# Kernel tuning notes

Measured on AMD Instinct MI355X. Metric: run time of the kernel, lower is better.

Reference implementation:

```python
import jax, jax.numpy as jnp
import numpy as np


def _add_self_loops(edge_index, num_nodes):
    loops = jnp.arange(num_nodes, dtype=edge_index.dtype)
    row = jnp.concatenate([edge_index[0], loops])
    col = jnp.concatenate([edge_index[1], loops])
    return row, col


def _gcn_norm(row, col, num_nodes):
    # deg computed at aggregation targets (col), edge weights all 1 (PyG gcn_norm)
    deg = jax.ops.segment_sum(jnp.ones_like(col, dtype=jnp.float32), col,
                              num_segments=num_nodes)
    dinv = jnp.where(deg > 0, jax.lax.rsqrt(deg), 0.0)
    return dinv[row] * dinv[col]  # [E+N]


def _gcn_conv(x, row, col, norm, W, b, num_nodes):
    h = x @ W                                  # [N, out] linear first (PyG GCNConv)
    msg = h[row] * norm[:, None]               # gather + scale, [E+N, out]
    agg = jax.ops.segment_sum(msg, col, num_segments=num_nodes)
    return agg + b


def setup_inputs() -> dict:
    key = jax.random.key(0)
    N, F, H, E = 100000, 128, 64, 1600000
    k1, k2, k3, k4 = jax.random.split(key, 4)
    x = jax.random.normal(k1, (N, F), dtype=jnp.float32)
    edge_index = jax.random.randint(k2, (2, E), 0, N, dtype=jnp.int64)
    s1 = 1.0 / np.sqrt(F)
    s2 = 1.0 / np.sqrt(H)
    W1 = jax.random.normal(k3, (F, H), dtype=jnp.float32) * s1
    b1 = jnp.zeros((H,), dtype=jnp.float32)
    W2 = jax.random.normal(k4, (H, 1), dtype=jnp.float32) * s2
    b2 = jnp.zeros((1,), dtype=jnp.float32)
    return {"x": x, "edge_index": edge_index, "W1": W1, "b1": b1,
            "W2": W2, "b2": b2}


def reference(x, edge_index, W1, b1, W2, b2):
    N = x.shape[0]
    row, col = _add_self_loops(edge_index, N)
    norm = _gcn_norm(row, col, N)
    h = jax.nn.relu(_gcn_conv(x, row, col, norm, W1, b1, N))
    # dropout p=0.0 -> identity
    out = _gcn_conv(h, row, col, norm, W2, b2, N)
    return out.reshape(-1)  # [N]
```

## Files before the change

kernel.cpp:

```cpp
#include <hip/hip_runtime.h>
#include <hip/hip_bf16.h>


#define SHIFT 9
#define BMASK ((1 << SHIFT) - 1)

typedef __attribute__((ext_vector_type(8))) short bf16x8;
typedef __attribute__((ext_vector_type(4))) float f32x4;

__device__ __forceinline__ bool detect_i64(const unsigned* u) {
    unsigned acc = 0;
#pragma unroll
    for (int i = 1; i <= 32; ++i) acc |= u[2 * i + 1];
    return acc == 0u;
}

__device__ __forceinline__ int load_edge(const void* ei, bool is64, long long idx) {
    if (is64) return ((const int*)ei)[idx << 1];
    return ((const int*)ei)[idx];
}

__device__ __forceinline__ unsigned bf16_rn(float x) {
    unsigned u = __float_as_uint(x);
    return (u + 0x7fffu + ((u >> 16) & 1u)) >> 16;
}
__device__ __forceinline__ unsigned pack_bf2(float a, float b) {
    return bf16_rn(a) | (bf16_rn(b) << 16);
}
__device__ __forceinline__ float bflo(unsigned v) { return __uint_as_float(v << 16); }
__device__ __forceinline__ float bfhi(unsigned v) {
    return __uint_as_float(v & 0xffff0000u);
}

__global__ __launch_bounds__(256) void binA_kernel(const void* ei, int* gcursor,
                                                   unsigned* __restrict__ pairs, int E,
                                                   int cap) {
    bool is64 = detect_i64((const unsigned*)ei);
    __shared__ int whist[4][256];
    __shared__ int bcur[256];
    int t = threadIdx.x;
    int wid = t >> 6;
    long long per = ((long long)E + gridDim.x - 1) / gridDim.x;
    long long e0 = (long long)blockIdx.x * per;
    long long e1 = e0 + per;
    if (e1 > E) e1 = E;
    whist[0][t] = 0; whist[1][t] = 0; whist[2][t] = 0; whist[3][t] = 0;
    __syncthreads();
    for (long long e = e0 + t; e < e1; e += 256) {
        int c = load_edge(ei, is64, (long long)E + e);
        atomicAdd(&whist[wid][c >> SHIFT], 1);
    }
    __syncthreads();
    int tot = whist[0][t] + whist[1][t] + whist[2][t] + whist[3][t];
    int rel = tot ? atomicAdd(&gcursor[t], tot) : 0;
    bcur[t] = t * cap + rel;
    __syncthreads();
    for (long long e = e0 + t; e < e1; e += 256) {
        int r = load_edge(ei, is64, e);
        int c = load_edge(ei, is64, (long long)E + e);
        int b = c >> SHIFT;
        int rk = atomicAdd(&bcur[b], 1);
        pairs[rk] = ((unsigned)r << SHIFT) | (unsigned)(c & BMASK);
    }
}

__global__ __launch_bounds__(256) void binB_kernel(const unsigned* __restrict__ pairs,
                                                   const int* __restrict__ gcursor,
                                                   int* __restrict__ csr,
                                                   int* __restrict__ offs,
                                                   int* __restrict__ deg, int N,
                                                   int cap) {
    __shared__ int cnt[1 << SHIFT];
    __shared__ int cur[1 << SHIFT];
    __shared__ int tmp[256];
    int b = blockIdx.x, t = threadIdx.x;
    int start = b * cap, end = b * cap + gcursor[b];
    cnt[t] = 0;
    cnt[t + 256] = 0;
    __syncthreads();
    for (int i = start + t; i < end; i += 256) atomicAdd(&cnt[pairs[i] & BMASK], 1);
    __syncthreads();
    int c0 = cnt[2 * t], c1 = cnt[2 * t + 1];
    int s = c0 + c1;
    tmp[t] = s;
    __syncthreads();
    for (int off = 1; off < 256; off <<= 1) {
        int xv = (t >= off) ? tmp[t - off] : 0;
        __syncthreads();
        tmp[t] += xv;
        __syncthreads();
    }
    int excl = tmp[t] - s;
    int p0 = start + excl;
    int p1 = p0 + c0;
    cur[2 * t] = p0;
    cur[2 * t + 1] = p1;
    int node0 = (b << SHIFT) + 2 * t;
    if (node0 < N) { offs[node0] = p0; deg[node0] = c0; }
    if (node0 + 1 < N) { offs[node0 + 1] = p1; deg[node0 + 1] = c1; }
    __syncthreads();
    for (int i = start + t; i < end; i += 256) {
        unsigned p = pairs[i];
        int pos = atomicAdd(&cur[p & BMASK], 1);
        csr[pos] = (int)(p >> SHIFT);
    }
}

__global__ __launch_bounds__(256) void gemm1_kernel(const float* __restrict__ x,
                                                    const float* __restrict__ W1,
                                                    const int* __restrict__ deg,
                                                    unsigned* __restrict__ hs_u, int N) {
    __shared__ alignas(16) char smem[32768];
    char* wt_hi = smem;
    char* wt_lo = smem + 16384;
    int t = threadIdx.x;
    int l = t & 63;
    int w = t >> 6;

#pragma unroll
    for (int i = 0; i < 32; ++i) {
        int idx = t + 256 * i;
        int k = idx >> 6;
        int c = idx & 63;
        float f = W1[idx];
        unsigned uh = bf16_rn(f);
        float fh = __uint_as_float(uh << 16);
        unsigned ul = bf16_rn(f - fh);
        int byte = c * 256 + (((k >> 3) ^ (c & 15)) << 4) + ((k & 7) << 1);
        *(unsigned short*)(wt_hi + byte) = (unsigned short)uh;
        *(unsigned short*)(wt_lo + byte) = (unsigned short)ul;
    }
    __syncthreads();

    int row0 = blockIdx.x * 64 + w * 16;
    int arow = row0 + (l & 15);
    bool rok = arow < N;
    const f32x4* x4 = (const f32x4*)x;

    f32x4 acc[4];
#pragma unroll
    for (int ct = 0; ct < 4; ++ct) acc[ct] = (f32x4)(0.f);

#pragma unroll
    for (int ks = 0; ks < 4; ++ks) {
        int kbase = ks * 32 + (l >> 4) * 8;
        f32x4 xa = (f32x4)(0.f), xb = (f32x4)(0.f);
        if (rok) {
            xa = x4[(size_t)arow * 32 + (kbase >> 2)];
            xb = x4[(size_t)arow * 32 + (kbase >> 2) + 1];
        }
        unsigned ah[4], al[4];
#pragma unroll
        for (int j = 0; j < 4; ++j) {
            float f0 = (j < 2) ? ((j == 0) ? xa.x : xa.z) : ((j == 2) ? xb.x : xb.z);
            float f1 = (j < 2) ? ((j == 0) ? xa.y : xa.w) : ((j == 2) ? xb.y : xb.w);
            unsigned h0 = bf16_rn(f0), h1 = bf16_rn(f1);
            float r0 = f0 - __uint_as_float(h0 << 16);
            float r1 = f1 - __uint_as_float(h1 << 16);
            ah[j] = h0 | (h1 << 16);
            al[j] = bf16_rn(r0) | (bf16_rn(r1) << 16);
        }
        bf16x8 Ah, Al;
        ((unsigned*)&Ah)[0] = ah[0]; ((unsigned*)&Ah)[1] = ah[1];
        ((unsigned*)&Ah)[2] = ah[2]; ((unsigned*)&Ah)[3] = ah[3];
        ((unsigned*)&Al)[0] = al[0]; ((unsigned*)&Al)[1] = al[1];
        ((unsigned*)&Al)[2] = al[2]; ((unsigned*)&Al)[3] = al[3];
        int chunk = ks * 4 + (l >> 4);
#pragma unroll
        for (int ct = 0; ct < 4; ++ct) {
            int col = ct * 16 + (l & 15);
            int byte = col * 256 + ((chunk ^ (col & 15)) << 4);
            bf16x8 Bh = *(const bf16x8*)(wt_hi + byte);
            bf16x8 Bl = *(const bf16x8*)(wt_lo + byte);
            acc[ct] = __builtin_amdgcn_mfma_f32_16x16x32_bf16(Ah, Bh, acc[ct], 0, 0, 0);
            acc[ct] = __builtin_amdgcn_mfma_f32_16x16x32_bf16(Ah, Bl, acc[ct], 0, 0, 0);
            acc[ct] = __builtin_amdgcn_mfma_f32_16x16x32_bf16(Al, Bh, acc[ct], 0, 0, 0);
        }
    }

    __syncthreads();
    float* hsb = (float*)(smem) + w * 16 * 68;
#pragma unroll
    for (int ct = 0; ct < 4; ++ct) {
#pragma unroll
        for (int i = 0; i < 4; ++i) {
            int row = (l >> 4) * 4 + i;
            hsb[row * 68 + ct * 16 + (l & 15)] = acc[ct][i];
        }
    }
    __syncthreads();
    int row = l & 15;
    int q = l >> 4;
    int gr = row0 + row;
    if (gr < N) {
        float dinv = rsqrtf((float)deg[gr] + 1.0f);
        const f32x4* src = (const f32x4*)(hsb + row * 68 + q * 16);
        f32x4 f0 = src[0], f1 = src[1], f2 = src[2], f3 = src[3];
        uint4 o0, o1;
        o0.x = pack_bf2(f0.x * dinv, f0.y * dinv);
        o0.y = pack_bf2(f0.z * dinv, f0.w * dinv);
        o0.z = pack_bf2(f1.x * dinv, f1.y * dinv);
        o0.w = pack_bf2(f1.z * dinv, f1.w * dinv);
        o1.x = pack_bf2(f2.x * dinv, f2.y * dinv);
        o1.y = pack_bf2(f2.z * dinv, f2.w * dinv);
        o1.z = pack_bf2(f3.x * dinv, f3.y * dinv);
        o1.w = pack_bf2(f3.z * dinv, f3.w * dinv);
        uint4* dst = (uint4*)&hs_u[(size_t)gr * 32 + q * 8];
        dst[0] = o0;
        dst[1] = o1;
    }
}

#define ACCV(v)                                            \
    {                                                      \
        float2 t0 = make_float2(bflo((v).x), bfhi((v).x)); \
        float2 t1 = make_float2(bflo((v).y), bfhi((v).y)); \
        float2 t2 = make_float2(bflo((v).z), bfhi((v).z)); \
        float2 t3 = make_float2(bflo((v).w), bfhi((v).w)); \
        a0.x += t0.x; a0.y += t0.y;                        \
        a1.x += t1.x; a1.y += t1.y;                        \
        a2.x += t2.x; a2.y += t2.y;                        \
        a3.x += t3.x; a3.y += t3.y;                        \
    }

__global__ __launch_bounds__(256) void pull1_kernel(
    const uint4* __restrict__ hs4, const int* __restrict__ offs,
    const int* __restrict__ deg, const int* __restrict__ csr,
    const float* __restrict__ b1, const float* __restrict__ W2,
    float* __restrict__ hs2, int N) {
    int gid = blockIdx.x * blockDim.x + threadIdx.x;
    int w = gid >> 3;
    if (w >= N) return;
    int lane = threadIdx.x & 63;
    int k = lane & 7;
    int s = offs[w];
    int cnt = deg[w];
    float dinv = rsqrtf((float)cnt + 1.0f);
    float2 a0 = make_float2(0.f, 0.f), a1 = a0, a2 = a0, a3 = a0;
    {
        uint4 v = hs4[(size_t)w * 8 + k];
        ACCV(v);
    }
    int e = 0;
    for (; e + 8 <= cnt; e += 8) {
        int r0 = csr[s + e + 0];
        int r1 = csr[s + e + 1];
        int r2 = csr[s + e + 2];
        int r3 = csr[s + e + 3];
        int r4 = csr[s + e + 4];
        int r5 = csr[s + e + 5];
        int r6 = csr[s + e + 6];
        int r7 = csr[s + e + 7];
        uint4 v0 = hs4[(size_t)r0 * 8 + k];
        uint4 v1 = hs4[(size_t)r1 * 8 + k];
        uint4 v2 = hs4[(size_t)r2 * 8 + k];
        uint4 v3 = hs4[(size_t)r3 * 8 + k];
        uint4 v4 = hs4[(size_t)r4 * 8 + k];
        uint4 v5 = hs4[(size_t)r5 * 8 + k];
        uint4 v6 = hs4[(size_t)r6 * 8 + k];
        uint4 v7 = hs4[(size_t)r7 * 8 + k];
        ACCV(v0); ACCV(v1); ACCV(v2); ACCV(v3);
        ACCV(v4); ACCV(v5); ACCV(v6); ACCV(v7);
    }
    for (; e < cnt; ++e) {
        int r = csr[s + e];
        uint4 v = hs4[(size_t)r * 8 + k];
        ACCV(v);
    }
    float4 bA = ((const float4*)b1)[2 * k];
    float4 bB = ((const float4*)b1)[2 * k + 1];
    float4 wA = ((const float4*)W2)[2 * k];
    float4 wB = ((const float4*)W2)[2 * k + 1];
    float p = fmaxf(fmaf(dinv, a0.x, bA.x), 0.f) * wA.x
            + fmaxf(fmaf(dinv, a0.y, bA.y), 0.f) * wA.y
            + fmaxf(fmaf(dinv, a1.x, bA.z), 0.f) * wA.z
            + fmaxf(fmaf(dinv, a1.y, bA.w), 0.f) * wA.w
            + fmaxf(fmaf(dinv, a2.x, bB.x), 0.f) * wB.x
            + fmaxf(fmaf(dinv, a2.y, bB.y), 0.f) * wB.y
            + fmaxf(fmaf(dinv, a3.x, bB.z), 0.f) * wB.z
            + fmaxf(fmaf(dinv, a3.y, bB.w), 0.f) * wB.w;
    p += __shfl_xor(p, 1);
    p += __shfl_xor(p, 2);
    p += __shfl_xor(p, 4);
    if ((lane & 7) == 0) hs2[w] = dinv * p;
}

__global__ __launch_bounds__(256) void pull2_kernel(
    const float* __restrict__ hs2, const int* __restrict__ offs,
    const int* __restrict__ deg, const int* __restrict__ csr,
    const float* __restrict__ b2, float* __restrict__ out, int N) {
    int i = blockIdx.x * blockDim.x + threadIdx.x;
    if (i >= N) return;
    int s = offs[i];
    int cnt = deg[i];
    float dinv = rsqrtf((float)cnt + 1.0f);
    float a0 = hs2[i];
    float a1 = 0.f, a2 = 0.f, a3 = 0.f;
    int kk = 0;
    for (; kk + 4 <= cnt; kk += 4) {
        a0 += hs2[csr[s + kk]];
        a1 += hs2[csr[s + kk + 1]];
        a2 += hs2[csr[s + kk + 2]];
        a3 += hs2[csr[s + kk + 3]];
    }
    for (; kk < cnt; ++kk) a0 += hs2[csr[s + kk]];
    out[i] = fmaf(dinv, (a0 + a1) + (a2 + a3), b2[0]);
}

extern "C" void kernel_launch(void* const* d_in, const int* in_sizes, int n_in,
                              void* d_out, int out_size, void* d_ws, size_t ws_size,
                              hipStream_t stream) {
    const float* x = (const float*)d_in[0];
    const void* ei = d_in[1];
    const float* W1 = (const float*)d_in[2];
    const float* b1 = (const float*)d_in[3];
    const float* W2 = (const float*)d_in[4];
    const float* b2 = (const float*)d_in[5];
    float* out = (float*)d_out;

    int N = in_sizes[0] / 128;
    int E = in_sizes[1] / 2;
    int NB = (N + (1 << SHIFT) - 1) >> SHIFT;
    int cap = ((2 * (E / NB)) / 256 + 2) * 256;

    char* p = (char*)d_ws;
    unsigned* hs_u = (unsigned*)p;  p += (size_t)N * 32 * sizeof(unsigned);
    float* hs2 = (float*)p;         p += (size_t)N * sizeof(float);
    int* offs = (int*)p;            p += (size_t)N * sizeof(int);
    int* deg = (int*)p;             p += (size_t)N * sizeof(int);
    unsigned* pairs = (unsigned*)p; p += (size_t)NB * cap * sizeof(unsigned);
    int* csr = (int*)p;             p += (size_t)NB * cap * sizeof(int);
    int* gcursor = (int*)p;         p += 256 * sizeof(int);

    (void)hipMemsetAsync(gcursor, 0, 256 * sizeof(int), stream);
    binA_kernel<<<512, 256, 0, stream>>>(ei, gcursor, pairs, E, cap);
    binB_kernel<<<NB, 256, 0, stream>>>(pairs, gcursor, csr, offs, deg, N, cap);
    gemm1_kernel<<<(N + 63) / 64, 256, 0, stream>>>(x, W1, deg, hs_u, N);
    pull1_kernel<<<((size_t)N * 8 + 255) / 256, 256, 0, stream>>>(
        (const uint4*)hs_u, offs, deg, csr, b1, W2, hs2, N);
    pull2_kernel<<<(N + 255) / 256, 256, 0, stream>>>(hs2, offs, deg, csr, b2, out, N);
}
```

Measured before the change: 199.0 us.

## Use finer dst bins, cache edges in registers during binning, unroll pull2 by 8

Bucket size drops from 512 to 256 nodes, which doubles the number of bins (up to 512) and gives one node per thread in the binB scan. binA now loads each edge once, caching up to 16 packed edges per thread in registers between the histogram pass and the scatter pass instead of reloading edge_index. pull2 unrolls its neighbor gather loop to 8 independent accumulators to expose more memory-level parallelism. The cost is more registers in binA, more global cursor atomics, and more, smaller binB blocks.

```diff
diff --git a/kernel.cpp b/kernel.cpp
--- a/kernel.cpp
+++ b/kernel.cpp
@@ -2,8 +2,9 @@
 #include <hip/hip_bf16.h>
 
 
-#define SHIFT 9
+#define SHIFT 8
 #define BMASK ((1 << SHIFT) - 1)
+#define MAXB 512
 
 typedef __attribute__((ext_vector_type(8))) short bf16x8;
 typedef __attribute__((ext_vector_type(4))) float f32x4;
@@ -34,33 +35,53 @@
 
 __global__ __launch_bounds__(256) void binA_kernel(const void* ei, int* gcursor,
                                                    unsigned* __restrict__ pairs, int E,
-                                                   int cap) {
+                                                   int cap, int NB) {
     bool is64 = detect_i64((const unsigned*)ei);
-    __shared__ int whist[4][256];
-    __shared__ int bcur[256];
+    __shared__ int whist[4][MAXB];
+    __shared__ int bcur[MAXB];
     int t = threadIdx.x;
     int wid = t >> 6;
     long long per = ((long long)E + gridDim.x - 1) / gridDim.x;
     long long e0 = (long long)blockIdx.x * per;
     long long e1 = e0 + per;
     if (e1 > E) e1 = E;
-    whist[0][t] = 0; whist[1][t] = 0; whist[2][t] = 0; whist[3][t] = 0;
-    __syncthreads();
-    for (long long e = e0 + t; e < e1; e += 256) {
-        int c = load_edge(ei, is64, (long long)E + e);
-        atomicAdd(&whist[wid][c >> SHIFT], 1);
-    }
-    __syncthreads();
-    int tot = whist[0][t] + whist[1][t] + whist[2][t] + whist[3][t];
-    int rel = tot ? atomicAdd(&gcursor[t], tot) : 0;
-    bcur[t] = t * cap + rel;
-    __syncthreads();
-    for (long long e = e0 + t; e < e1; e += 256) {
+    for (int b = t; b < NB; b += 256) {
+        whist[0][b] = 0; whist[1][b] = 0; whist[2][b] = 0; whist[3][b] = 0;
+    }
+    __syncthreads();
+    unsigned pk[16];
+    int bs[16];
+    int i = 0;
+    for (long long e = e0 + t; e < e1; e += 256, ++i) {
         int r = load_edge(ei, is64, e);
         int c = load_edge(ei, is64, (long long)E + e);
         int b = c >> SHIFT;
+        unsigned p = ((unsigned)r << SHIFT) | (unsigned)(c & BMASK);
+        atomicAdd(&whist[wid][b], 1);
+        if (i < 16) { pk[i] = p; bs[i] = b; }
+    }
+    __syncthreads();
+    for (int b = t; b < NB; b += 256) {
+        int tot = whist[0][b] + whist[1][b] + whist[2][b] + whist[3][b];
+        int rel = tot ? atomicAdd(&gcursor[b], tot) : 0;
+        bcur[b] = b * cap + rel;
+    }
+    __syncthreads();
+    i = 0;
+    for (long long e = e0 + t; e < e1; e += 256, ++i) {
+        unsigned p;
+        int b;
+        if (i < 16) {
+            p = pk[i];
+            b = bs[i];
+        } else {
+            int r = load_edge(ei, is64, e);
+            int c = load_edge(ei, is64, (long long)E + e);
+            b = c >> SHIFT;
+            p = ((unsigned)r << SHIFT) | (unsigned)(c & BMASK);
+        }
         int rk = atomicAdd(&bcur[b], 1);
-        pairs[rk] = ((unsigned)r << SHIFT) | (unsigned)(c & BMASK);
+        pairs[rk] = p;
     }
 }
 
@@ -70,19 +91,17 @@
                                                    int* __restrict__ offs,
                                                    int* __restrict__ deg, int N,
                                                    int cap) {
-    __shared__ int cnt[1 << SHIFT];
-    __shared__ int cur[1 << SHIFT];
+    __shared__ int cnt[256];
+    __shared__ int cur[256];
     __shared__ int tmp[256];
     int b = blockIdx.x, t = threadIdx.x;
-    int start = b * cap, end = b * cap + gcursor[b];
+    int start = b * cap, end = start + gcursor[b];
     cnt[t] = 0;
-    cnt[t + 256] = 0;
     __syncthreads();
     for (int i = start + t; i < end; i += 256) atomicAdd(&cnt[pairs[i] & BMASK], 1);
     __syncthreads();
-    int c0 = cnt[2 * t], c1 = cnt[2 * t + 1];
-    int s = c0 + c1;
-    tmp[t] = s;
+    int c0 = cnt[t];
+    tmp[t] = c0;
     __syncthreads();
     for (int off = 1; off < 256; off <<= 1) {
         int xv = (t >= off) ? tmp[t - off] : 0;
@@ -90,14 +109,13 @@
         tmp[t] += xv;
         __syncthreads();
     }
-    int excl = tmp[t] - s;
-    int p0 = start + excl;
-    int p1 = p0 + c0;
-    cur[2 * t] = p0;
-    cur[2 * t + 1] = p1;
-    int node0 = (b << SHIFT) + 2 * t;
-    if (node0 < N) { offs[node0] = p0; deg[node0] = c0; }
-    if (node0 + 1 < N) { offs[node0 + 1] = p1; deg[node0 + 1] = c1; }
+    int p0 = start + tmp[t] - c0;
+    cur[t] = p0;
+    int node = (b << SHIFT) + t;
+    if (node < N) {
+        offs[node] = p0;
+        deg[node] = c0;
+    }
     __syncthreads();
     for (int i = start + t; i < end; i += 256) {
         unsigned p = pairs[i];
@@ -296,15 +314,20 @@
     float dinv = rsqrtf((float)cnt + 1.0f);
     float a0 = hs2[i];
     float a1 = 0.f, a2 = 0.f, a3 = 0.f;
+    float a4 = 0.f, a5 = 0.f, a6 = 0.f, a7 = 0.f;
     int kk = 0;
-    for (; kk + 4 <= cnt; kk += 4) {
+    for (; kk + 8 <= cnt; kk += 8) {
         a0 += hs2[csr[s + kk]];
         a1 += hs2[csr[s + kk + 1]];
         a2 += hs2[csr[s + kk + 2]];
         a3 += hs2[csr[s + kk + 3]];
+        a4 += hs2[csr[s + kk + 4]];
+        a5 += hs2[csr[s + kk + 5]];
+        a6 += hs2[csr[s + kk + 6]];
+        a7 += hs2[csr[s + kk + 7]];
     }
     for (; kk < cnt; ++kk) a0 += hs2[csr[s + kk]];
-    out[i] = fmaf(dinv, (a0 + a1) + (a2 + a3), b2[0]);
+    out[i] = fmaf(dinv, ((a0 + a1) + (a2 + a3)) + ((a4 + a5) + (a6 + a7)), b2[0]);
 }
 
 extern "C" void kernel_launch(void* const* d_in, const int* in_sizes, int n_in,
@@ -330,10 +353,10 @@
     int* deg = (int*)p;             p += (size_t)N * sizeof(int);
     unsigned* pairs = (unsigned*)p; p += (size_t)NB * cap * sizeof(unsigned);
     int* csr = (int*)p;             p += (size_t)NB * cap * sizeof(int);
-    int* gcursor = (int*)p;         p += 256 * sizeof(int);
-
-    (void)hipMemsetAsync(gcursor, 0, 256 * sizeof(int), stream);
-    binA_kernel<<<512, 256, 0, stream>>>(ei, gcursor, pairs, E, cap);
+    int* gcursor = (int*)p;         p += MAXB * sizeof(int);
+
+    (void)hipMemsetAsync(gcursor, 0, MAXB * sizeof(int), stream);
+    binA_kernel<<<512, 256, 0, stream>>>(ei, gcursor, pairs, E, cap, NB);
     binB_kernel<<<NB, 256, 0, stream>>>(pairs, gcursor, csr, offs, deg, N, cap);
     gemm1_kernel<<<(N + 63) / 64, 256, 0, stream>>>(x, W1, deg, hs_u, N);
     pull1_kernel<<<((size_t)N * 8 + 255) / 256, 256, 0, stream>>>(
```

Result: faster. 192.8 us (-3.1%).
